# Kernel tuning notes

Measured on AMD Instinct MI355X. Metric: run time of the kernel, lower is better.

## Reference

```python
import jax, jax.numpy as jnp
import numpy as np

S = 128            # dense volume side used to build sparse topology
N = 500_000        # active voxels per grid
C = 8              # channels (SparseConv3d(8, 8, 3))
K = 27             # 3x3x3 kernel taps


def _build_neighbor_map(seed):
    """Sample N unique voxels from an S^3 volume; return [N,27] neighbor index map, -1 = missing."""
    rng = np.random.default_rng(seed)
    flat = rng.choice(S ** 3, size=N, replace=False)
    lut = np.full(S ** 3, -1, dtype=np.int32)
    lut[flat] = np.arange(N, dtype=np.int32)
    x = flat // (S * S)
    y = (flat // S) % S
    z = flat % S
    coords = np.stack([x, y, z], axis=1).astype(np.int64)          # [N,3]
    offs = np.array(list(np.ndindex(3, 3, 3)), dtype=np.int64) - 1  # [27,3]
    nc = coords[:, None, :] + offs[None, :, :]                      # [N,27,3]
    valid = ((nc >= 0) & (nc < S)).all(-1)
    ncl = np.clip(nc, 0, S - 1)
    nflat = ncl[..., 0] * S * S + ncl[..., 1] * S + ncl[..., 2]
    return np.where(valid, lut[nflat], -1).astype(np.int32)


def setup_inputs() -> dict:
    key = jax.random.key(0)
    k0, k1, k2, k3 = jax.random.split(key, 4)
    feats0 = jax.random.normal(k0, (N, C), jnp.float32)
    feats1 = jax.random.normal(k1, (N, C), jnp.float32)
    # xavier_uniform for a [3,3,3,8,8] conv weight: fan_in = fan_out = 27*8
    bound = float(np.sqrt(6.0 / (K * C + K * C)))
    W0 = jax.random.uniform(k2, (3, K, C, C), jnp.float32, -bound, bound)
    W1 = jax.random.uniform(k3, (3, K, C, C), jnp.float32, -bound, bound)
    nbr0 = jnp.asarray(_build_neighbor_map(1))
    nbr1 = jnp.asarray(_build_neighbor_map(2))
    return {"feats0": feats0, "feats1": feats1, "W0": W0, "W1": W1,
            "nbr0": nbr0, "nbr1": nbr1}


def _sparse_conv(x, w, nbr, mask):
    # gather-GEMM: x [N,C], w [K,C,C], nbr [N,K] (-1 -> masked zero)
    g = jnp.where(mask[..., None], x[jnp.maximum(nbr, 0)], 0.0)  # [N,K,C]
    return jnp.einsum('nkc,kcd->nd', g, w)


def _grid_forward(x0, W, nbr):
    # conv -> relu -> conv -> relu -> conv -> + residual (per grid)
    mask = nbr >= 0
    x = jax.nn.relu(_sparse_conv(x0, W[0], nbr, mask))
    x = jax.nn.relu(_sparse_conv(x, W[1], nbr, mask))
    x = _sparse_conv(x, W[2], nbr, mask)
    return x + x0


def reference(feats0, feats1, W0, W1, nbr0, nbr1):
    out0 = _grid_forward(feats0, W0, nbr0)
    out1 = _grid_forward(feats1, W1, nbr1)
    return jnp.concatenate([out0, out1], axis=0)  # fvdb.jcat of per-grid results
```

## Files before the change

kernel.cpp:

```cpp
#include <hip/hip_runtime.h>
#include <stdint.h>

#define C 8
#define K 27
#define BLOCK 256
#define VPT 2
#define WSZ (K * C * C)

__device__ __forceinline__ uint32_t pack_bf2(float a, float b) {
    uint32_t ua = __float_as_uint(a);
    uint32_t ub = __float_as_uint(b);
    ua = (ua + 0x7FFFu + ((ua >> 16) & 1u)) >> 16;
    ub = (ub + 0x7FFFu + ((ub >> 16) & 1u)) & 0xFFFF0000u;
    return ua | ub;
}

__global__ __launch_bounds__(BLOCK) void to_bf16_kernel(
    const float4* __restrict__ x, uint4* __restrict__ t, int n)
{
    int i = blockIdx.x * BLOCK + threadIdx.x;
    if (i >= n) return;
    float4 a = x[(size_t)i * 2], b = x[(size_t)i * 2 + 1];
    uint4 o;
    o.x = pack_bf2(a.x, a.y);
    o.y = pack_bf2(a.z, a.w);
    o.z = pack_bf2(b.x, b.y);
    o.w = pack_bf2(b.z, b.w);
    t[i] = o;
}

__global__ __launch_bounds__(BLOCK) void transpose_nbr_kernel(
    const int* __restrict__ nbr, int* __restrict__ nbrT, int n)
{
    int i = blockIdx.x * BLOCK + threadIdx.x;
    if (i >= n) return;
#pragma unroll
    for (int k = 0; k < K; ++k)
        nbrT[(size_t)k * n + i] = nbr[(size_t)i * K + k];
}

template<int RELU, int OUTBF16, int NBRT>
__global__ __launch_bounds__(BLOCK) void sconv_kernel(
    const uint4* __restrict__ xt, const float* __restrict__ Wl,
    const int* __restrict__ nb, const float* __restrict__ resid,
    void* __restrict__ yout, int n)
{
    __shared__ float w_lds[WSZ];
    for (int i = threadIdx.x; i < WSZ; i += BLOCK) w_lds[i] = Wl[i];
    __syncthreads();

    int vox[VPT];
    float acc[VPT][C];
#pragma unroll
    for (int v = 0; v < VPT; ++v) {
        vox[v] = blockIdx.x * (BLOCK * VPT) + v * BLOCK + threadIdx.x;
#pragma unroll
        for (int d = 0; d < C; ++d) acc[v][d] = 0.f;
    }

#pragma unroll 1
    for (int k = 0; k < K; ++k) {
        uint4 g[VPT];
#pragma unroll
        for (int v = 0; v < VPT; ++v) {
            int id = -1;
            if (vox[v] < n)
                id = NBRT ? nb[(size_t)k * n + vox[v]]
                          : nb[(size_t)vox[v] * K + k];
            g[v] = (id >= 0) ? xt[id] : make_uint4(0u, 0u, 0u, 0u);
        }
        const float4* wk = (const float4*)(w_lds + k * C * C);
#pragma unroll
        for (int c = 0; c < C; ++c) {
            float4 wlo = wk[c * 2], whi = wk[c * 2 + 1];
#pragma unroll
            for (int v = 0; v < VPT; ++v) {
                uint32_t w32 = (&g[v].x)[c >> 1];
                float a = (c & 1) ? __uint_as_float(w32 & 0xFFFF0000u)
                                  : __uint_as_float(w32 << 16);
                acc[v][0] += a * wlo.x; acc[v][1] += a * wlo.y;
                acc[v][2] += a * wlo.z; acc[v][3] += a * wlo.w;
                acc[v][4] += a * whi.x; acc[v][5] += a * whi.y;
                acc[v][6] += a * whi.z; acc[v][7] += a * whi.w;
            }
        }
    }

#pragma unroll
    for (int v = 0; v < VPT; ++v) {
        if (vox[v] >= n) continue;
#pragma unroll
        for (int d = 0; d < C; ++d)
            if (RELU) acc[v][d] = fmaxf(acc[v][d], 0.f);
        if (OUTBF16) {
            uint4 o;
            o.x = pack_bf2(acc[v][0], acc[v][1]);
            o.y = pack_bf2(acc[v][2], acc[v][3]);
            o.z = pack_bf2(acc[v][4], acc[v][5]);
            o.w = pack_bf2(acc[v][6], acc[v][7]);
            ((uint4*)yout)[vox[v]] = o;
        } else {
            float4 o0 = make_float4(acc[v][0], acc[v][1], acc[v][2], acc[v][3]);
            float4 o1 = make_float4(acc[v][4], acc[v][5], acc[v][6], acc[v][7]);
            const float4* r = (const float4*)(resid + (size_t)vox[v] * C);
            float4 r0 = r[0], r1 = r[1];
            o0.x += r0.x; o0.y += r0.y; o0.z += r0.z; o0.w += r0.w;
            o1.x += r1.x; o1.y += r1.y; o1.z += r1.z; o1.w += r1.w;
            float4* yp = (float4*)((float*)yout + (size_t)vox[v] * C);
            yp[0] = o0; yp[1] = o1;
        }
    }
}

extern "C" void kernel_launch(void* const* d_in, const int* in_sizes, int n_in,
                              void* d_out, int out_size, void* d_ws, size_t ws_size,
                              hipStream_t stream) {
    const float* feats0 = (const float*)d_in[0];
    const float* feats1 = (const float*)d_in[1];
    const float* W0     = (const float*)d_in[2];
    const float* W1     = (const float*)d_in[3];
    const int*   nbr0   = (const int*)d_in[4];
    const int*   nbr1   = (const int*)d_in[5];
    float* out = (float*)d_out;

    const int n = in_sizes[0] / C;
    uint4* bufA = (uint4*)d_ws;
    uint4* bufB = bufA + n;
    size_t tbl_bytes = (size_t)n * 16 * 2;
    int* nbrT = (int*)((char*)d_ws + tbl_bytes);
    const bool useT = ws_size >= tbl_bytes + (size_t)n * K * 4;

    dim3 blk(BLOCK);
    int gridc = (n + BLOCK - 1) / BLOCK;
    int gridv = (n + BLOCK * VPT - 1) / (BLOCK * VPT);

    for (int g = 0; g < 2; ++g) {
        const float* x0  = g ? feats1 : feats0;
        const float* Wg  = g ? W1 : W0;
        const int*   nbr = g ? nbr1 : nbr0;
        float* og = out + (size_t)g * n * C;

        to_bf16_kernel<<<gridc, blk, 0, stream>>>((const float4*)x0, bufA, n);
        if (useT) {
            transpose_nbr_kernel<<<gridc, blk, 0, stream>>>(nbr, nbrT, n);
            sconv_kernel<1, 1, 1><<<gridv, blk, 0, stream>>>(bufA, Wg,            nbrT, nullptr, bufB, n);
            sconv_kernel<1, 1, 1><<<gridv, blk, 0, stream>>>(bufB, Wg + WSZ,      nbrT, nullptr, bufA, n);
            sconv_kernel<0, 0, 1><<<gridv, blk, 0, stream>>>(bufA, Wg + 2 * WSZ,  nbrT, x0,      og,   n);
        } else {
            sconv_kernel<1, 1, 0><<<gridv, blk, 0, stream>>>(bufA, Wg,            nbr,  nullptr, bufB, n);
            sconv_kernel<1, 1, 0><<<gridv, blk, 0, stream>>>(bufB, Wg + WSZ,      nbr,  nullptr, bufA, n);
            sconv_kernel<0, 0, 0><<<gridv, blk, 0, stream>>>(bufA, Wg + 2 * WSZ,  nbr,  x0,      og,   n);
        }
    }
}
```

Before: 472.5 us.

## Compact neighbor map into CSR of valid taps and iterate only active neighbors

Builds a per-voxel compacted list of valid (tap, neighbor) pairs using an atomic counter, then each conv layer iterates only over valid entries with a software-prefetched gather. This removes the reads and FMAs spent on the roughly three quarters of taps that are missing. It drops the VPT=2 multi-voxel per thread scheme and pads the weight LDS rows. The cost is variable per-thread loop lengths, which cause wavefront divergence, dependent entry-then-feature loads, and a fixed entry capacity cap.

```diff
diff --git a/kernel.cpp b/kernel.cpp
--- a/kernel.cpp
+++ b/kernel.cpp
@@ -4,8 +4,9 @@
 #define C 8
 #define K 27
 #define BLOCK 256
-#define VPT 2
+#define WSTRIDE 66
 #define WSZ (K * C * C)
+#define ENTRY_CAP (1u << 22)
 
 __device__ __forceinline__ uint32_t pack_bf2(float a, float b) {
     uint32_t ua = __float_as_uint(a);
@@ -29,86 +30,150 @@
     t[i] = o;
 }
 
-__global__ __launch_bounds__(BLOCK) void transpose_nbr_kernel(
-    const int* __restrict__ nbr, int* __restrict__ nbrT, int n)
-{
-    int i = blockIdx.x * BLOCK + threadIdx.x;
-    if (i >= n) return;
-#pragma unroll
-    for (int k = 0; k < K; ++k)
-        nbrT[(size_t)k * n + i] = nbr[(size_t)i * K + k];
-}
-
-template<int RELU, int OUTBF16, int NBRT>
-__global__ __launch_bounds__(BLOCK) void sconv_kernel(
+__global__ void zero_ctr_kernel(uint32_t* ctr) {
+    if (threadIdx.x == 0 && blockIdx.x == 0) *ctr = 0;
+}
+
+__global__ __launch_bounds__(BLOCK) void build_csr_kernel(
+    const int* __restrict__ nbr, uint32_t* __restrict__ off,
+    uint32_t* __restrict__ entries, uint32_t* __restrict__ ctr, int n)
+{
+    int i = blockIdx.x * BLOCK + threadIdx.x;
+    if (i >= n) return;
+    uint32_t tmp[K];
+    int cnt = 0;
+#pragma unroll
+    for (int k = 0; k < K; ++k) {
+        int idx = nbr[(size_t)i * K + k];
+        if (idx >= 0) tmp[cnt++] = ((uint32_t)k << 19) | (uint32_t)idx;
+    }
+    uint32_t base = atomicAdd(ctr, (uint32_t)cnt);
+    off[i] = base | ((uint32_t)cnt << 27);
+    if (base + (uint32_t)cnt <= ENTRY_CAP)
+        for (int j = 0; j < cnt; ++j) entries[base + j] = tmp[j];
+}
+
+template<int RELU, int OUTBF16>
+__global__ __launch_bounds__(BLOCK) void sconv_csr_kernel(
     const uint4* __restrict__ xt, const float* __restrict__ Wl,
-    const int* __restrict__ nb, const float* __restrict__ resid,
+    const uint32_t* __restrict__ off, const uint32_t* __restrict__ entries,
+    const float* __restrict__ resid, void* __restrict__ yout, int n)
+{
+    __shared__ float w_lds[K * WSTRIDE];
+    for (int t = threadIdx.x; t < WSZ; t += BLOCK) {
+        int k = t >> 6, r = t & 63;
+        w_lds[k * WSTRIDE + r] = Wl[t];
+    }
+    __syncthreads();
+
+    int i = blockIdx.x * BLOCK + threadIdx.x;
+    if (i >= n) return;
+
+    uint32_t o = off[i];
+    uint32_t base = o & 0x7FFFFFFu;
+    int cnt = (int)(o >> 27);
+
+    float acc[C];
+#pragma unroll
+    for (int d = 0; d < C; ++d) acc[d] = 0.f;
+
+    uint32_t e = 0;
+    uint4 g = make_uint4(0u, 0u, 0u, 0u);
+    if (cnt > 0) {
+        e = entries[base];
+        g = xt[e & 0x7FFFFu];
+    }
+    for (int j = 0; j < cnt; ++j) {
+        uint32_t e_n = 0;
+        uint4 g_n = make_uint4(0u, 0u, 0u, 0u);
+        if (j + 1 < cnt) {
+            e_n = entries[base + j + 1];
+            g_n = xt[e_n & 0x7FFFFu];
+        }
+        const float* wk = w_lds + (e >> 19) * WSTRIDE;
+#pragma unroll
+        for (int c = 0; c < C; ++c) {
+            uint32_t w32 = (&g.x)[c >> 1];
+            float a = (c & 1) ? __uint_as_float(w32 & 0xFFFF0000u)
+                              : __uint_as_float(w32 << 16);
+#pragma unroll
+            for (int d = 0; d < C; ++d) acc[d] += a * wk[c * 8 + d];
+        }
+        e = e_n;
+        g = g_n;
+    }
+
+#pragma unroll
+    for (int d = 0; d < C; ++d)
+        if (RELU) acc[d] = fmaxf(acc[d], 0.f);
+
+    if (OUTBF16) {
+        uint4 ov;
+        ov.x = pack_bf2(acc[0], acc[1]);
+        ov.y = pack_bf2(acc[2], acc[3]);
+        ov.z = pack_bf2(acc[4], acc[5]);
+        ov.w = pack_bf2(acc[6], acc[7]);
+        ((uint4*)yout)[i] = ov;
+    } else {
+        const float4* r = (const float4*)(resid + (size_t)i * C);
+        float4 r0 = r[0], r1 = r[1];
+        float4 o0 = make_float4(acc[0] + r0.x, acc[1] + r0.y, acc[2] + r0.z, acc[3] + r0.w);
+        float4 o1 = make_float4(acc[4] + r1.x, acc[5] + r1.y, acc[6] + r1.z, acc[7] + r1.w);
+        float4* yp = (float4*)((float*)yout + (size_t)i * C);
+        yp[0] = o0;
+        yp[1] = o1;
+    }
+}
+
+template<int RELU, int OUTBF16>
+__global__ __launch_bounds__(BLOCK) void sconv_dense_kernel(
+    const uint4* __restrict__ xt, const float* __restrict__ Wl,
+    const int* __restrict__ nbr, const float* __restrict__ resid,
     void* __restrict__ yout, int n)
 {
     __shared__ float w_lds[WSZ];
-    for (int i = threadIdx.x; i < WSZ; i += BLOCK) w_lds[i] = Wl[i];
+    for (int t = threadIdx.x; t < WSZ; t += BLOCK) w_lds[t] = Wl[t];
     __syncthreads();
-
-    int vox[VPT];
-    float acc[VPT][C];
-#pragma unroll
-    for (int v = 0; v < VPT; ++v) {
-        vox[v] = blockIdx.x * (BLOCK * VPT) + v * BLOCK + threadIdx.x;
-#pragma unroll
-        for (int d = 0; d < C; ++d) acc[v][d] = 0.f;
-    }
-
+    int i = blockIdx.x * BLOCK + threadIdx.x;
+    if (i >= n) return;
+    float acc[C];
+#pragma unroll
+    for (int d = 0; d < C; ++d) acc[d] = 0.f;
 #pragma unroll 1
     for (int k = 0; k < K; ++k) {
-        uint4 g[VPT];
-#pragma unroll
-        for (int v = 0; v < VPT; ++v) {
-            int id = -1;
-            if (vox[v] < n)
-                id = NBRT ? nb[(size_t)k * n + vox[v]]
-                          : nb[(size_t)vox[v] * K + k];
-            g[v] = (id >= 0) ? xt[id] : make_uint4(0u, 0u, 0u, 0u);
-        }
+        int idx = nbr[(size_t)i * K + k];
+        uint4 g = (idx >= 0) ? xt[idx] : make_uint4(0u, 0u, 0u, 0u);
         const float4* wk = (const float4*)(w_lds + k * C * C);
 #pragma unroll
         for (int c = 0; c < C; ++c) {
             float4 wlo = wk[c * 2], whi = wk[c * 2 + 1];
-#pragma unroll
-            for (int v = 0; v < VPT; ++v) {
-                uint32_t w32 = (&g[v].x)[c >> 1];
-                float a = (c & 1) ? __uint_as_float(w32 & 0xFFFF0000u)
-                                  : __uint_as_float(w32 << 16);
-                acc[v][0] += a * wlo.x; acc[v][1] += a * wlo.y;
-                acc[v][2] += a * wlo.z; acc[v][3] += a * wlo.w;
-                acc[v][4] += a * whi.x; acc[v][5] += a * whi.y;
-                acc[v][6] += a * whi.z; acc[v][7] += a * whi.w;
-            }
-        }
-    }
-
-#pragma unroll
-    for (int v = 0; v < VPT; ++v) {
-        if (vox[v] >= n) continue;
-#pragma unroll
-        for (int d = 0; d < C; ++d)
-            if (RELU) acc[v][d] = fmaxf(acc[v][d], 0.f);
-        if (OUTBF16) {
-            uint4 o;
-            o.x = pack_bf2(acc[v][0], acc[v][1]);
-            o.y = pack_bf2(acc[v][2], acc[v][3]);
-            o.z = pack_bf2(acc[v][4], acc[v][5]);
-            o.w = pack_bf2(acc[v][6], acc[v][7]);
-            ((uint4*)yout)[vox[v]] = o;
-        } else {
-            float4 o0 = make_float4(acc[v][0], acc[v][1], acc[v][2], acc[v][3]);
-            float4 o1 = make_float4(acc[v][4], acc[v][5], acc[v][6], acc[v][7]);
-            const float4* r = (const float4*)(resid + (size_t)vox[v] * C);
-            float4 r0 = r[0], r1 = r[1];
-            o0.x += r0.x; o0.y += r0.y; o0.z += r0.z; o0.w += r0.w;
-            o1.x += r1.x; o1.y += r1.y; o1.z += r1.z; o1.w += r1.w;
-            float4* yp = (float4*)((float*)yout + (size_t)vox[v] * C);
-            yp[0] = o0; yp[1] = o1;
-        }
+            uint32_t w32 = (&g.x)[c >> 1];
+            float a = (c & 1) ? __uint_as_float(w32 & 0xFFFF0000u)
+                              : __uint_as_float(w32 << 16);
+            acc[0] += a * wlo.x; acc[1] += a * wlo.y;
+            acc[2] += a * wlo.z; acc[3] += a * wlo.w;
+            acc[4] += a * whi.x; acc[5] += a * whi.y;
+            acc[6] += a * whi.z; acc[7] += a * whi.w;
+        }
+    }
+#pragma unroll
+    for (int d = 0; d < C; ++d)
+        if (RELU) acc[d] = fmaxf(acc[d], 0.f);
+    if (OUTBF16) {
+        uint4 ov;
+        ov.x = pack_bf2(acc[0], acc[1]);
+        ov.y = pack_bf2(acc[2], acc[3]);
+        ov.z = pack_bf2(acc[4], acc[5]);
+        ov.w = pack_bf2(acc[6], acc[7]);
+        ((uint4*)yout)[i] = ov;
+    } else {
+        const float4* r = (const float4*)(resid + (size_t)i * C);
+        float4 r0 = r[0], r1 = r[1];
+        float4 o0 = make_float4(acc[0] + r0.x, acc[1] + r0.y, acc[2] + r0.z, acc[3] + r0.w);
+        float4 o1 = make_float4(acc[4] + r1.x, acc[5] + r1.y, acc[6] + r1.z, acc[7] + r1.w);
+        float4* yp = (float4*)((float*)yout + (size_t)i * C);
+        yp[0] = o0;
+        yp[1] = o1;
     }
 }
 
@@ -124,15 +189,18 @@
     float* out = (float*)d_out;
 
     const int n = in_sizes[0] / C;
-    uint4* bufA = (uint4*)d_ws;
-    uint4* bufB = bufA + n;
-    size_t tbl_bytes = (size_t)n * 16 * 2;
-    int* nbrT = (int*)((char*)d_ws + tbl_bytes);
-    const bool useT = ws_size >= tbl_bytes + (size_t)n * K * 4;
+
+    char* ws = (char*)d_ws;
+    uint4* bufA = (uint4*)ws;
+    uint4* bufB = (uint4*)(ws + (size_t)n * 16);
+    uint32_t* offs = (uint32_t*)(ws + (size_t)n * 32);
+    uint32_t* ctr  = (uint32_t*)(ws + (size_t)n * 36);
+    uint32_t* entries = (uint32_t*)(ws + (size_t)n * 36 + 64);
+    const size_t need = (size_t)n * 36 + 64 + (size_t)ENTRY_CAP * 4;
+    const bool use_csr = ws_size >= need;
 
     dim3 blk(BLOCK);
-    int gridc = (n + BLOCK - 1) / BLOCK;
-    int gridv = (n + BLOCK * VPT - 1) / (BLOCK * VPT);
+    int grid1 = (n + BLOCK - 1) / BLOCK;
 
     for (int g = 0; g < 2; ++g) {
         const float* x0  = g ? feats1 : feats0;
@@ -140,16 +208,17 @@
         const int*   nbr = g ? nbr1 : nbr0;
         float* og = out + (size_t)g * n * C;
 
-        to_bf16_kernel<<<gridc, blk, 0, stream>>>((const float4*)x0, bufA, n);
-        if (useT) {
-            transpose_nbr_kernel<<<gridc, blk, 0, stream>>>(nbr, nbrT, n);
-            sconv_kernel<1, 1, 1><<<gridv, blk, 0, stream>>>(bufA, Wg,            nbrT, nullptr, bufB, n);
-            sconv_kernel<1, 1, 1><<<gridv, blk, 0, stream>>>(bufB, Wg + WSZ,      nbrT, nullptr, bufA, n);
-            sconv_kernel<0, 0, 1><<<gridv, blk, 0, stream>>>(bufA, Wg + 2 * WSZ,  nbrT, x0,      og,   n);
+        to_bf16_kernel<<<grid1, blk, 0, stream>>>((const float4*)x0, bufA, n);
+        if (use_csr) {
+            zero_ctr_kernel<<<1, 64, 0, stream>>>(ctr);
+            build_csr_kernel<<<grid1, blk, 0, stream>>>(nbr, offs, entries, ctr, n);
+            sconv_csr_kernel<1, 1><<<grid1, blk, 0, stream>>>(bufA, Wg,           offs, entries, nullptr, bufB, n);
+            sconv_csr_kernel<1, 1><<<grid1, blk, 0, stream>>>(bufB, Wg + WSZ,     offs, entries, nullptr, bufA, n);
+            sconv_csr_kernel<0, 0><<<grid1, blk, 0, stream>>>(bufA, Wg + 2 * WSZ, offs, entries, x0,      og,   n);
         } else {
-            sconv_kernel<1, 1, 0><<<gridv, blk, 0, stream>>>(bufA, Wg,            nbr,  nullptr, bufB, n);
-            sconv_kernel<1, 1, 0><<<gridv, blk, 0, stream>>>(bufB, Wg + WSZ,      nbr,  nullptr, bufA, n);
-            sconv_kernel<0, 0, 0><<<gridv, blk, 0, stream>>>(bufA, Wg + 2 * WSZ,  nbr,  x0,      og,   n);
-        }
-    }
-}
+            sconv_dense_kernel<1, 1><<<grid1, blk, 0, stream>>>(bufA, Wg,           nbr, nullptr, bufB, n);
+            sconv_dense_kernel<1, 1><<<grid1, blk, 0, stream>>>(bufB, Wg + WSZ,     nbr, nullptr, bufA, n);
+            sconv_dense_kernel<0, 0><<<grid1, blk, 0, stream>>>(bufA, Wg + 2 * WSZ, nbr, x0,      og,   n);
+        }
+    }
+}
```

Result: slower. 771.9 us (+63.4%).
